# Performance work log

Measured on AMD Instinct MI355X. Metric: run time of the kernel, lower is better.

Reference implementation:

```python
import jax, jax.numpy as jnp
import numpy as np

T, B, N, D, O = 500, 64, 512, 100, 10
ALPHA = 0.1


def setup_inputs() -> dict:
    key = jax.random.key(0)
    ks = jax.random.split(key, 13)
    sN = 1.0 / np.sqrt(N)
    sD = 1.0 / np.sqrt(D)
    return {
        "X": jax.random.normal(ks[0], (T, B, D), jnp.float32),
        "W_rec_m1": jax.random.normal(ks[1], (N, N), jnp.float32) * sN,
        "W_rec_pmd": jax.random.normal(ks[2], (N, N), jnp.float32) * sN,
        "W_rec_s1": jax.random.normal(ks[3], (N, N), jnp.float32) * sN,
        "b_m1": jnp.zeros((N,), jnp.float32),
        "b_pmd": jnp.zeros((N,), jnp.float32),
        "b_s1": jnp.zeros((N,), jnp.float32),
        "W_pmd_m1": jax.random.normal(ks[4], (N, N), jnp.float32) * sN,
        "W_s1_m1": jax.random.normal(ks[5], (N, N), jnp.float32) * sN,
        "W_m1_pmd": jax.random.normal(ks[6], (N, N), jnp.float32) * sN,
        "W_in_pmd": jax.random.normal(ks[7], (N, D), jnp.float32) * sD,
        "W_in_s1": jax.random.normal(ks[8], (N, D), jnp.float32) * sD,
        "W_out": jax.random.normal(ks[9], (O, N), jnp.float32) * sN,
    }


def reference(X, W_rec_m1, W_rec_pmd, W_rec_s1, b_m1, b_pmd, b_s1,
              W_pmd_m1, W_s1_m1, W_m1_pmd, W_in_pmd, W_in_s1, W_out):
    a = jnp.float32(ALPHA)

    def step(carry, Xt):
        x_m1, x_pmd, x_s1, r_m1, r_pmd, r_s1 = carry
        # message passing: accumulate inputs to each region
        in_m1 = r_pmd @ W_pmd_m1.T + r_s1 @ W_s1_m1.T            # [B, N]
        in_pmd = r_m1 @ W_m1_pmd.T + Xt @ W_in_pmd.T             # [B, N]
        in_s1 = Xt @ W_in_s1.T                                   # [B, N]
        # leaky-RNN f_step per region
        x_m1 = (1 - a) * x_m1 + a * (r_m1 @ W_rec_m1.T + in_m1 + b_m1)
        x_pmd = (1 - a) * x_pmd + a * (r_pmd @ W_rec_pmd.T + in_pmd + b_pmd)
        x_s1 = (1 - a) * x_s1 + a * (r_s1 @ W_rec_s1.T + in_s1 + b_s1)
        r_m1, r_pmd, r_s1 = jnp.tanh(x_m1), jnp.tanh(x_pmd), jnp.tanh(x_s1)
        out_t = r_m1 @ W_out.T                                   # [B, O]
        return (x_m1, x_pmd, x_s1, r_m1, r_pmd, r_s1), (out_t, r_m1, r_pmd, r_s1)

    z = jnp.zeros((B, N), X.dtype)
    init = (z, z, z, z, z, z)  # zero hidden; rates[0] = tanh(0) = 0
    _, (out, r_m1, r_pmd, r_s1) = jax.lax.scan(step, init, X[1:])
    return out  # [T-1, B, O]
```

## Files before the change

### kernel.cpp

```cpp
#include <hip/hip_runtime.h>
#include <hip/hip_cooperative_groups.h>

namespace cg = cooperative_groups;

#define NT 499
#define NB 64
#define NN 512
#define ND 100
#define NO 10
#define NWAVE 16
#define KW 32
#define NWG 256

#define XT_SZ   (NT * ND * NB)
#define RBUF_SZ (2 * NN * NB)
#define XT_OFF  0
#define RM_OFF  (XT_OFF + XT_SZ)
#define RP_OFF  (RM_OFF + RBUF_SZ)
#define RS_OFF  (RP_OFF + RBUF_SZ)
#define FLAG_OFF (RS_OFF + RBUF_SZ)
#define WPK_OFF  (FLAG_OFF + 8192)
#define RPK_STRIDE ((NN / 2) * NB)
#define WMAT (NN * (NN / 2))

__device__ __forceinline__ void st_cg_u(unsigned* p, unsigned v) {
  __hip_atomic_store(p, v, __ATOMIC_RELAXED, __HIP_MEMORY_SCOPE_AGENT);
}

#define LD1(dst, base, voff, IMM) \
  asm volatile("global_load_dword %0, %1, %2 offset:" IMM " sc0 sc1" \
               : "=v"(dst) : "v"(voff), "s"(base))
#define LDR(u, base, voff) do { \
  LD1(u[0],  base, voff, "0");    LD1(u[1],  base, voff, "256");  \
  LD1(u[2],  base, voff, "512");  LD1(u[3],  base, voff, "768");  \
  LD1(u[4],  base, voff, "1024"); LD1(u[5],  base, voff, "1280"); \
  LD1(u[6],  base, voff, "1536"); LD1(u[7],  base, voff, "1792"); \
  LD1(u[8],  base, voff, "2048"); LD1(u[9],  base, voff, "2304"); \
  LD1(u[10], base, voff, "2560"); LD1(u[11], base, voff, "2816"); \
  LD1(u[12], base, voff, "3072"); LD1(u[13], base, voff, "3328"); \
  LD1(u[14], base, voff, "3584"); LD1(u[15], base, voff, "3840"); \
} while (0)

#define LD_SC(dst, addr) \
  asm volatile("global_load_dword %0, %1, off sc0 sc1" : "=v"(dst) : "v"(addr))

#define DOT2(acc, a, w) \
  asm("v_dot2_f32_f16 %0, %1, %2, %0" : "+v"(acc) : "v"(a), "s"(w))

__device__ __forceinline__ unsigned f2h2(float a, float b) {
  union { _Float16 h[2]; unsigned u; } cv;
  cv.h[0] = (_Float16)a; cv.h[1] = (_Float16)b;
  return cv.u;
}

__global__ void xpose_kernel(const float* __restrict__ X, float* __restrict__ XT) {
  __shared__ float tile[NB * ND];
  const int t = blockIdx.x;
  const float* src = X + (size_t)(t + 1) * NB * ND;
  for (int i = threadIdx.x; i < NB * ND; i += blockDim.x) tile[i] = src[i];
  __syncthreads();
  float* dst = XT + (size_t)t * ND * NB;
  for (int i = threadIdx.x; i < NB * ND; i += blockDim.x) {
    const int d = i >> 6, b = i & 63;
    dst[i] = tile[b * ND + d];
  }
}

__global__ void wpack_kernel(const float* __restrict__ W_rec_m1,
                             const float* __restrict__ W_m1_pmd,
                             const float* __restrict__ W_pmd_m1,
                             const float* __restrict__ W_rec_pmd,
                             const float* __restrict__ W_s1_m1,
                             const float* __restrict__ W_rec_s1,
                             const float* __restrict__ W_out,
                             unsigned* __restrict__ WPK) {
  const int idx = blockIdx.x, t = threadIdx.x;
  const float* src; unsigned* dst;
  if (idx < 6 * NN) {
    const int mat = idx >> 9, row = idx & (NN - 1);
    const float* m[6] = {W_rec_m1, W_m1_pmd, W_pmd_m1, W_rec_pmd, W_s1_m1, W_rec_s1};
    src = m[mat] + (size_t)row * NN;
    dst = WPK + (size_t)mat * WMAT + (size_t)row * (NN / 2);
  } else {
    const int row = idx - 6 * NN;
    src = W_out + (size_t)row * NN;
    dst = WPK + (size_t)6 * WMAT + (size_t)row * (NN / 2);
  }
  union { _Float16 h[2]; unsigned u; } cv;
  cv.h[0] = (_Float16)src[2 * t];
  cv.h[1] = (_Float16)src[2 * t + 1];
  dst[t] = cv.u;
}

__global__ void __launch_bounds__(1024, 4)
rnn_kernel(const float* __restrict__ XT,
           unsigned* __restrict__ rmPK, unsigned* __restrict__ rpPK,
           unsigned* __restrict__ rsPK,
           const unsigned* __restrict__ WPK,
           const float* __restrict__ b_m1, const float* __restrict__ b_pmd,
           const float* __restrict__ b_s1,
           const float* __restrict__ W_in_pmd, const float* __restrict__ W_in_s1,
           float* __restrict__ out,
           unsigned* __restrict__ flags)
{
  const int g    = blockIdx.x;
  const int grp  = g >> 4;
  const int wave = __builtin_amdgcn_readfirstlane((int)threadIdx.x >> 6);
  const int lane = (int)threadIdx.x & 63;
  const int n0 = 2 * g, n1 = 2 * g + 1;
  const int m0 = __builtin_amdgcn_readfirstlane(wave * (KW / 2));
  const int d0 = __builtin_amdgcn_readfirstlane(wave * 7);
  int dlen = ND - d0; dlen = dlen < 0 ? 0 : (dlen > 7 ? 7 : dlen);
  const bool has_out = (g < NO);
  const unsigned voff = (unsigned)lane * 4u;

  __shared__ float red[NWAVE][7][64];

  for (int i = g * (int)blockDim.x + (int)threadIdx.x; i < RPK_STRIDE;
       i += (int)(gridDim.x * blockDim.x)) {
    rmPK[i] = 0u; rpPK[i] = 0u; rsPK[i] = 0u;
  }
  if (g <= 16 && threadIdx.x == 0) flags[g * 16] = 0u;

  const unsigned* wrm0b = WPK + (size_t)0 * WMAT + (size_t)n0 * (NN / 2) + m0;
  const unsigned* wrm1b = WPK + (size_t)0 * WMAT + (size_t)n1 * (NN / 2) + m0;
  const unsigned* wmp0b = WPK + (size_t)1 * WMAT + (size_t)n0 * (NN / 2) + m0;
  const unsigned* wmp1b = WPK + (size_t)1 * WMAT + (size_t)n1 * (NN / 2) + m0;
  const unsigned* wpm0b = WPK + (size_t)2 * WMAT + (size_t)n0 * (NN / 2) + m0;
  const unsigned* wpm1b = WPK + (size_t)2 * WMAT + (size_t)n1 * (NN / 2) + m0;
  const unsigned* wrp0b = WPK + (size_t)3 * WMAT + (size_t)n0 * (NN / 2) + m0;
  const unsigned* wrp1b = WPK + (size_t)3 * WMAT + (size_t)n1 * (NN / 2) + m0;
  const unsigned* wsm0b = WPK + (size_t)4 * WMAT + (size_t)n0 * (NN / 2) + m0;
  const unsigned* wsm1b = WPK + (size_t)4 * WMAT + (size_t)n1 * (NN / 2) + m0;
  const unsigned* wrs0b = WPK + (size_t)5 * WMAT + (size_t)n0 * (NN / 2) + m0;
  const unsigned* wrs1b = WPK + (size_t)5 * WMAT + (size_t)n1 * (NN / 2) + m0;
  const unsigned* wob   = WPK + (size_t)6 * WMAT
                              + (size_t)(has_out ? g : 0) * (NN / 2) + m0;
  const float* wip0 = W_in_pmd + (size_t)n0 * ND + d0;
  const float* wip1 = W_in_pmd + (size_t)n1 * ND + d0;
  const float* wis0 = W_in_s1 + (size_t)n0 * ND + d0;
  const float* wis1 = W_in_s1 + (size_t)n1 * ND + d0;

  unsigned* pubPK = nullptr; float bP0 = 0.f, bP1 = 0.f;
  if (wave == 0)      { pubPK = rmPK; bP0 = b_m1[n0];  bP1 = b_m1[n1]; }
  else if (wave == 1) { pubPK = rpPK; bP0 = b_pmd[n0]; bP1 = b_pmd[n1]; }
  else if (wave == 2) { pubPK = rsPK; bP0 = b_s1[n0];  bP1 = b_s1[n1]; }
  float xP0 = 0.f, xP1 = 0.f;

  float apX0 = 0.f, apX1 = 0.f, asX0 = 0.f, asX1 = 0.f;
  {
    const float* xt = XT + d0 * NB + lane;
    for (int d = 0; d < dlen; ++d) {
      const float v = xt[d * NB];
      apX0 = fmaf(v, wip0[d], apX0);
      apX1 = fmaf(v, wip1[d], apX1);
      asX0 = fmaf(v, wis0[d], asX0);
      asX1 = fmaf(v, wis1[d], asX1);
    }
  }

  cg::this_grid().sync();

  for (int ti = 0; ti < NT; ++ti) {
    const int cur = ti & 1, nxt = cur ^ 1;
    const unsigned* bM = rmPK + cur * RPK_STRIDE + m0 * NB;
    const unsigned* bP = rpPK + cur * RPK_STRIDE + m0 * NB;
    const unsigned* bS = rsPK + cur * RPK_STRIDE + m0 * NB;

    unsigned um[16], uP[16], uS[16];
    LDR(um, bM, voff);
    LDR(uP, bP, voff);
    LDR(uS, bS, voff);
    asm volatile("s_waitcnt vmcnt(0)" ::: "memory");
    __builtin_amdgcn_sched_barrier(0);

    float am0 = 0.f, am1 = 0.f;
    float ap0 = apX0, ap1 = apX1, as0 = asX0, as1 = asX1;

    #pragma unroll
    for (int j = 0; j < 16; ++j) {
      DOT2(am0, um[j], wrm0b[j]);
      DOT2(am1, um[j], wrm1b[j]);
      DOT2(ap0, um[j], wmp0b[j]);
      DOT2(ap1, um[j], wmp1b[j]);
    }
    #pragma unroll
    for (int j = 0; j < 16; ++j) {
      DOT2(am0, uP[j], wpm0b[j]);
      DOT2(am1, uP[j], wpm1b[j]);
      DOT2(ap0, uP[j], wrp0b[j]);
      DOT2(ap1, uP[j], wrp1b[j]);
    }
    #pragma unroll
    for (int j = 0; j < 16; ++j) {
      DOT2(am0, uS[j], wsm0b[j]);
      DOT2(am1, uS[j], wsm1b[j]);
      DOT2(as0, uS[j], wrs0b[j]);
      DOT2(as1, uS[j], wrs1b[j]);
    }

    red[wave][0][lane] = am0; red[wave][1][lane] = am1;
    red[wave][2][lane] = ap0; red[wave][3][lane] = ap1;
    red[wave][4][lane] = as0; red[wave][5][lane] = as1;
    __syncthreads();

    if (wave < 3) {
      float s0 = red[0][2 * wave][lane], s1 = red[0][2 * wave + 1][lane];
      #pragma unroll
      for (int w = 1; w < NWAVE; ++w) {
        s0 += red[w][2 * wave][lane];
        s1 += red[w][2 * wave + 1][lane];
      }
      xP0 = 0.9f * xP0 + 0.1f * (s0 + bP0);
      xP1 = 0.9f * xP1 + 0.1f * (s1 + bP1);
      st_cg_u(pubPK + nxt * RPK_STRIDE + g * NB + lane,
              f2h2(tanhf(xP0), tanhf(xP1)));
    } else if (wave == 3 && has_out && ti >= 2) {
      float s = red[0][6][lane];
      #pragma unroll
      for (int w = 1; w < NWAVE; ++w) s += red[w][6][lane];
      out[(size_t)(ti - 2) * (NB * NO) + lane * NO + g] = s;
    }

    __syncthreads();
    const unsigned tgtc = (unsigned)(ti + 1) * 16u;
    if (threadIdx.x == 0) {
      const unsigned old = __hip_atomic_fetch_add(
          &flags[(grp + 1) * 16], 1u, __ATOMIC_RELAXED, __HIP_MEMORY_SCOPE_AGENT);
      if (old == tgtc - 1u) {
        __hip_atomic_fetch_add(&flags[0], 1u, __ATOMIC_RELAXED,
                               __HIP_MEMORY_SCOPE_AGENT);
      }
    }

    apX0 = 0.f; apX1 = 0.f; asX0 = 0.f; asX1 = 0.f;
    if (ti + 1 < NT) {
      const float* xt = XT + (size_t)(ti + 1) * ND * NB + d0 * NB + lane;
      for (int d = 0; d < dlen; ++d) {
        const float v = xt[d * NB];
        apX0 = fmaf(v, wip0[d], apX0);
        apX1 = fmaf(v, wip1[d], apX1);
        asX0 = fmaf(v, wis0[d], asX0);
        asX1 = fmaf(v, wis1[d], asX1);
      }
    }
    if (has_out) {
      float ao = 0.f;
      #pragma unroll
      for (int j = 0; j < 16; ++j) DOT2(ao, um[j], wob[j]);
      red[wave][6][lane] = ao;
    }

    if (threadIdx.x == 0) {
      while (__hip_atomic_load(&flags[0], __ATOMIC_RELAXED,
                               __HIP_MEMORY_SCOPE_AGENT) < tgtc)
        __builtin_amdgcn_s_sleep(1);
    }
    __syncthreads();
  }

  if (has_out) {
    if (wave == 3) {
      float s = red[0][6][lane];
      #pragma unroll
      for (int w = 1; w < NWAVE; ++w) s += red[w][6][lane];
      out[(size_t)(NT - 2) * (NB * NO) + lane * NO + g] = s;
    }
    __syncthreads();
    const unsigned* rmP = rmPK + (NT & 1) * RPK_STRIDE + m0 * NB + lane;
    unsigned um[16];
    #pragma unroll
    for (int k2 = 0; k2 < 16; ++k2) LD_SC(um[k2], rmP + k2 * NB);
    asm volatile("s_waitcnt vmcnt(0)" ::: "memory");
    __builtin_amdgcn_sched_barrier(0);
    float ao = 0.f;
    #pragma unroll
    for (int j = 0; j < 16; ++j) DOT2(ao, um[j], wob[j]);
    red[wave][6][lane] = ao;
    __syncthreads();
    if (wave == 3) {
      float t = red[0][6][lane];
      #pragma unroll
      for (int w = 1; w < NWAVE; ++w) t += red[w][6][lane];
      out[(size_t)(NT - 1) * (NB * NO) + lane * NO + g] = t;
    }
  }
}

extern "C" void kernel_launch(void* const* d_in, const int* in_sizes, int n_in,
                              void* d_out, int out_size, void* d_ws, size_t ws_size,
                              hipStream_t stream) {
  (void)in_sizes; (void)n_in; (void)out_size; (void)ws_size;
  const float* X         = (const float*)d_in[0];
  const float* W_rec_m1  = (const float*)d_in[1];
  const float* W_rec_pmd = (const float*)d_in[2];
  const float* W_rec_s1  = (const float*)d_in[3];
  const float* b_m1      = (const float*)d_in[4];
  const float* b_pmd     = (const float*)d_in[5];
  const float* b_s1      = (const float*)d_in[6];
  const float* W_pmd_m1  = (const float*)d_in[7];
  const float* W_s1_m1   = (const float*)d_in[8];
  const float* W_m1_pmd  = (const float*)d_in[9];
  const float* W_in_pmd  = (const float*)d_in[10];
  const float* W_in_s1   = (const float*)d_in[11];
  const float* W_out     = (const float*)d_in[12];
  float* out = (float*)d_out;

  float* wsf = (float*)d_ws;
  const float* XT = wsf + XT_OFF;
  float* XTw   = wsf + XT_OFF;
  unsigned* rmPK = (unsigned*)(wsf + RM_OFF);
  unsigned* rpPK = (unsigned*)(wsf + RP_OFF);
  unsigned* rsPK = (unsigned*)(wsf + RS_OFF);
  unsigned* flags = (unsigned*)(wsf + FLAG_OFF);
  unsigned* WPK   = (unsigned*)(wsf + WPK_OFF);

  xpose_kernel<<<NT, 256, 0, stream>>>(X, XTw);
  wpack_kernel<<<6 * NN + NO, 256, 0, stream>>>(
      W_rec_m1, W_m1_pmd, W_pmd_m1, W_rec_pmd, W_s1_m1, W_rec_s1, W_out, WPK);

  const unsigned* WPKc = WPK;
  void* args[12];
  args[0]  = (void*)&XT;
  args[1]  = (void*)&rmPK;  args[2]  = (void*)&rpPK; args[3]  = (void*)&rsPK;
  args[4]  = (void*)&WPKc;
  args[5]  = (void*)&b_m1;  args[6]  = (void*)&b_pmd; args[7]  = (void*)&b_s1;
  args[8]  = (void*)&W_in_pmd; args[9] = (void*)&W_in_s1;
  args[10] = (void*)&out;
  args[11] = (void*)&flags;
  hipLaunchCooperativeKernel((const void*)rnn_kernel, dim3(NWG), dim3(1024), args, 0, stream);
}
```

Measured before the change: 3.266 ms.

## Consolidate per-step reduction in wave 0 and drop second block barrier

Wave 0 now reduces all six partial sums, updates all three regions' state, publishes the packed rates and signals the grid flag itself after a vmcnt wait. This removes the second __syncthreads per timestep. The output-projection partials are double-buffered in shared memory so their reduction can safely move to wave 1 without that barrier. The spin-wait also drops s_sleep to react faster. The cost is that the reduction and tanh work is serialized onto one wave instead of three, and a busy spin adds memory traffic.

```diff
diff --git a/kernel.cpp b/kernel.cpp
--- a/kernel.cpp
+++ b/kernel.cpp
@@ -114,7 +114,7 @@
   const bool has_out = (g < NO);
   const unsigned voff = (unsigned)lane * 4u;
 
-  __shared__ float red[NWAVE][7][64];
+  __shared__ float red[NWAVE][8][64];
 
   for (int i = g * (int)blockDim.x + (int)threadIdx.x; i < RPK_STRIDE;
        i += (int)(gridDim.x * blockDim.x)) {
@@ -141,11 +141,10 @@
   const float* wis0 = W_in_s1 + (size_t)n0 * ND + d0;
   const float* wis1 = W_in_s1 + (size_t)n1 * ND + d0;
 
-  unsigned* pubPK = nullptr; float bP0 = 0.f, bP1 = 0.f;
-  if (wave == 0)      { pubPK = rmPK; bP0 = b_m1[n0];  bP1 = b_m1[n1]; }
-  else if (wave == 1) { pubPK = rpPK; bP0 = b_pmd[n0]; bP1 = b_pmd[n1]; }
-  else if (wave == 2) { pubPK = rsPK; bP0 = b_s1[n0];  bP1 = b_s1[n1]; }
-  float xP0 = 0.f, xP1 = 0.f;
+  const float bm0 = b_m1[n0],  bm1 = b_m1[n1];
+  const float bp0 = b_pmd[n0], bp1 = b_pmd[n1];
+  const float bs0 = b_s1[n0],  bs1 = b_s1[n1];
+  float xm0 = 0.f, xm1 = 0.f, xp0 = 0.f, xp1 = 0.f, xs0 = 0.f, xs1 = 0.f;
 
   float apX0 = 0.f, apX1 = 0.f, asX0 = 0.f, asX1 = 0.f;
   {
@@ -195,7 +194,7 @@
     for (int j = 0; j < 16; ++j) {
       DOT2(am0, uS[j], wsm0b[j]);
       DOT2(am1, uS[j], wsm1b[j]);
-      DOT2(as0, uS[j], wrs0b[j]);
+      DOT2(as0, uS[j], wsm1b == wrs0b ? wrs0b[j] : wrs0b[j]);
       DOT2(as1, uS[j], wrs1b[j]);
     }
 
@@ -204,33 +203,39 @@
     red[wave][4][lane] = as0; red[wave][5][lane] = as1;
     __syncthreads();
 
-    if (wave < 3) {
-      float s0 = red[0][2 * wave][lane], s1 = red[0][2 * wave + 1][lane];
+    const unsigned tgtc = (unsigned)(ti + 1) * 16u;
+    if (wave == 0) {
+      float s0 = red[0][0][lane], s1 = red[0][1][lane], s2 = red[0][2][lane];
+      float s3 = red[0][3][lane], s4 = red[0][4][lane], s5 = red[0][5][lane];
       #pragma unroll
       for (int w = 1; w < NWAVE; ++w) {
-        s0 += red[w][2 * wave][lane];
-        s1 += red[w][2 * wave + 1][lane];
+        s0 += red[w][0][lane]; s1 += red[w][1][lane]; s2 += red[w][2][lane];
+        s3 += red[w][3][lane]; s4 += red[w][4][lane]; s5 += red[w][5][lane];
       }
-      xP0 = 0.9f * xP0 + 0.1f * (s0 + bP0);
-      xP1 = 0.9f * xP1 + 0.1f * (s1 + bP1);
-      st_cg_u(pubPK + nxt * RPK_STRIDE + g * NB + lane,
-              f2h2(tanhf(xP0), tanhf(xP1)));
-    } else if (wave == 3 && has_out && ti >= 2) {
-      float s = red[0][6][lane];
-      #pragma unroll
-      for (int w = 1; w < NWAVE; ++w) s += red[w][6][lane];
+      xm0 = 0.9f * xm0 + 0.1f * (s0 + bm0);
+      xm1 = 0.9f * xm1 + 0.1f * (s1 + bm1);
+      xp0 = 0.9f * xp0 + 0.1f * (s2 + bp0);
+      xp1 = 0.9f * xp1 + 0.1f * (s3 + bp1);
+      xs0 = 0.9f * xs0 + 0.1f * (s4 + bs0);
+      xs1 = 0.9f * xs1 + 0.1f * (s5 + bs1);
+      st_cg_u(rmPK + nxt * RPK_STRIDE + g * NB + lane, f2h2(tanhf(xm0), tanhf(xm1)));
+      st_cg_u(rpPK + nxt * RPK_STRIDE + g * NB + lane, f2h2(tanhf(xp0), tanhf(xp1)));
+      st_cg_u(rsPK + nxt * RPK_STRIDE + g * NB + lane, f2h2(tanhf(xs0), tanhf(xs1)));
+      asm volatile("s_waitcnt vmcnt(0)" ::: "memory");
+      if (threadIdx.x == 0) {
+        const unsigned old = __hip_atomic_fetch_add(
+            &flags[(grp + 1) * 16], 1u, __ATOMIC_RELAXED, __HIP_MEMORY_SCOPE_AGENT);
+        if (old == tgtc - 1u) {
+          __hip_atomic_fetch_add(&flags[0], 1u, __ATOMIC_RELAXED,
+                                 __HIP_MEMORY_SCOPE_AGENT);
+        }
+      }
+    } else if (wave == 1 && has_out && ti >= 2) {
+      const int pOld = 6 + ((ti - 1) & 1);
+      float s = red[0][pOld][lane];
+      #pragma unroll
+      for (int w = 1; w < NWAVE; ++w) s += red[w][pOld][lane];
       out[(size_t)(ti - 2) * (NB * NO) + lane * NO + g] = s;
-    }
-
-    __syncthreads();
-    const unsigned tgtc = (unsigned)(ti + 1) * 16u;
-    if (threadIdx.x == 0) {
-      const unsigned old = __hip_atomic_fetch_add(
-          &flags[(grp + 1) * 16], 1u, __ATOMIC_RELAXED, __HIP_MEMORY_SCOPE_AGENT);
-      if (old == tgtc - 1u) {
-        __hip_atomic_fetch_add(&flags[0], 1u, __ATOMIC_RELAXED,
-                               __HIP_MEMORY_SCOPE_AGENT);
-      }
     }
 
     apX0 = 0.f; apX1 = 0.f; asX0 = 0.f; asX1 = 0.f;
@@ -248,22 +253,23 @@
       float ao = 0.f;
       #pragma unroll
       for (int j = 0; j < 16; ++j) DOT2(ao, um[j], wob[j]);
-      red[wave][6][lane] = ao;
+      red[wave][6 + (ti & 1)][lane] = ao;
     }
 
     if (threadIdx.x == 0) {
       while (__hip_atomic_load(&flags[0], __ATOMIC_RELAXED,
                                __HIP_MEMORY_SCOPE_AGENT) < tgtc)
-        __builtin_amdgcn_s_sleep(1);
+        ;
     }
     __syncthreads();
   }
 
   if (has_out) {
-    if (wave == 3) {
-      float s = red[0][6][lane];
-      #pragma unroll
-      for (int w = 1; w < NWAVE; ++w) s += red[w][6][lane];
+    if (wave == 1) {
+      const int pl = 6 + ((NT - 1) & 1);
+      float s = red[0][pl][lane];
+      #pragma unroll
+      for (int w = 1; w < NWAVE; ++w) s += red[w][pl][lane];
       out[(size_t)(NT - 2) * (NB * NO) + lane * NO + g] = s;
     }
     __syncthreads();
@@ -276,12 +282,12 @@
     float ao = 0.f;
     #pragma unroll
     for (int j = 0; j < 16; ++j) DOT2(ao, um[j], wob[j]);
-    red[wave][6][lane] = ao;
+    red[wave][7][lane] = ao;
     __syncthreads();
-    if (wave == 3) {
-      float t = red[0][6][lane];
-      #pragma unroll
-      for (int w = 1; w < NWAVE; ++w) t += red[w][6][lane];
+    if (wave == 1) {
+      float t = red[0][7][lane];
+      #pragma unroll
+      for (int w = 1; w < NWAVE; ++w) t += red[w][7][lane];
       out[(size_t)(NT - 1) * (NB * NO) + lane * NO + g] = t;
     }
   }
```

New measurement: 3.574 ms. 9.4% more time.
